# Kernel optimization log

Hardware: AMD Instinct MI355X
Metric: run time of the kernel (lower is better)

The kernel has to match this reference:

```python
import jax, jax.numpy as jnp
import numpy as np

EMB = 64
HEADS = 8
B = 4
T = 2048


def setup_inputs() -> dict:
    key = jax.random.key(0)
    ks = jax.random.split(key, 7)
    s = 0.05
    x = jax.random.normal(ks[0], (B, T, EMB), dtype=jnp.float32)
    y = jax.random.normal(ks[1], (B, T, EMB), dtype=jnp.float32)
    mask = jax.random.randint(ks[2], (1, T, T), 0, 2, dtype=jnp.int32)
    Wk = jax.random.normal(ks[3], (EMB, EMB * HEADS), dtype=jnp.float32) * s
    Wq = jax.random.normal(ks[4], (EMB, EMB * HEADS), dtype=jnp.float32) * s
    Wv = jax.random.normal(ks[5], (EMB, EMB * HEADS), dtype=jnp.float32) * s
    Wu = jax.random.normal(ks[6], (EMB * HEADS, EMB), dtype=jnp.float32) * s
    bu = jnp.zeros((EMB,), dtype=jnp.float32)
    return {"x": x, "y": y, "mask": mask, "Wk": Wk, "Wq": Wq, "Wv": Wv, "Wu": Wu, "bu": bu}


def reference(x, y, mask, Wk, Wq, Wv, Wu, bu):
    b, t_x, e = x.shape
    _, t_y, _ = y.shape
    h = HEADS
    # projections: each head gets full dim e (head_dim == emb in this module)
    k = (x @ Wk).reshape(b, t_x, h, e).transpose(0, 2, 1, 3)  # [b,h,t_x,e]
    q = (y @ Wq).reshape(b, t_y, h, e).transpose(0, 2, 1, 3)  # [b,h,t_y,e]
    v = (x @ Wv).reshape(b, t_x, h, e).transpose(0, 2, 1, 3)  # [b,h,t_x,e]
    scale = jnp.asarray(e, x.dtype) ** 0.25
    q = q / scale
    k = k / scale
    dot = jnp.einsum('bhqe,bhke->bhqk', q, k)  # [b,h,t_y,t_x]
    # mask: [1,t_y,t_x] broadcast over batch*heads; fill -1e9 where mask==0
    dot = jnp.where(mask[:, None, :, :] == 0, jnp.asarray(-1e9, dot.dtype), dot)
    att = jax.nn.softmax(dot, axis=-1)
    out = jnp.einsum('bhqk,bhke->bqhe', att, v).reshape(b, t_y, h * e)
    return out @ Wu + bu
```

## Files before the change

kernel.cpp:

```cpp
#include <hip/hip_runtime.h>

#define EMB 64
#define HEADS 8
#define SEQ 2048

typedef short short8 __attribute__((ext_vector_type(8)));
typedef float f32x4 __attribute__((ext_vector_type(4)));
typedef unsigned int u32;

__device__ __forceinline__ float4 ld4(const float* p) { return *(const float4*)p; }
__device__ __forceinline__ unsigned short f2bf(float f) {
  union { float f; unsigned u; } x; x.f = f;
  return (unsigned short)((x.u + 0x7fffu + ((x.u >> 16) & 1u)) >> 16);
}
__device__ __forceinline__ float bf2f(unsigned short s) {
  union { unsigned u; float f; } x; x.u = ((unsigned)s) << 16;
  return x.f;
}
__device__ __forceinline__ float bits2f(u32 u) {
  union { u32 u; float f; } x; x.u = u;
  return x.f;
}
__device__ __forceinline__ u32 cvtpk(float lo, float hi) {
  u32 r;
  asm("v_cvt_pk_bf16_f32 %0, %1, %2" : "=v"(r) : "v"(lo), "v"(hi));
  return r;
}
__device__ __forceinline__ float vexp2(float x) {
  float r;
  asm("v_exp_f32 %0, %1" : "=v"(r) : "v"(x));
  return r;
}
__device__ __forceinline__ void gload16(const void* g, void* l) {
  __builtin_amdgcn_global_load_lds((const __attribute__((address_space(1))) unsigned int*)g,
                                   (__attribute__((address_space(3))) unsigned int*)l, 16, 0, 0);
}

#define LOG2E 1.4426950408889634f
#define NC0  (-5.770780163555854f)

__global__ __launch_bounds__(256) void prep_kernel(
    const float* __restrict__ x, const float* __restrict__ y,
    const float* __restrict__ Wk, const float* __restrict__ Wq, const float* __restrict__ Wv,
    const int* __restrict__ mask, const float* __restrict__ Wu,
    unsigned short* __restrict__ Kbuf, unsigned short* __restrict__ Qbuf,
    unsigned short* __restrict__ VbufT, u32* __restrict__ pmask,
    unsigned short* __restrict__ WuThi, unsigned short* __restrict__ WuTlo)
{
  __shared__ alignas(16) char psmem[18688];
  const int t = threadIdx.x;
  const int z = blockIdx.z;

  if (z == 3) {
    int (*Ms)[68] = (int (*)[68])psmem;
    const int bid = blockIdx.x * 8 + blockIdx.y;
    const int qblk = bid >> 5, kt = bid & 31;
    #pragma unroll
    for (int j = 0; j < 4; ++j) {
      const int idx = t + j * 256;
      const int row = idx >> 4, col4 = (idx & 15) << 2;
      *(int4*)&Ms[row][col4] =
          *(const int4*)&mask[(size_t)(qblk*64 + row) * SEQ + kt*64 + col4];
    }
    __syncthreads();
    #pragma unroll
    for (int it = 0; it < 8; ++it) {
      const int gid = bid * 2048 + it * 256 + t;
      const int i = gid & 7, ll = (gid >> 3) & 63, ww = (gid >> 9) & 3;
      const int ql = ww*16 + (ll & 15);
      const int g = ll >> 4, c = i >> 1, rr = i & 1;
      const int kl = 16*c + 4*g + 2*rr;
      const int m0 = Ms[ql][kl], m1 = Ms[ql][kl + 1];
      pmask[gid] = (m0 ? 0xFFFFu : 0u) | (m1 ? 0xFFFF0000u : 0u);
    }
    if (blockIdx.y == 7) {
      const int idx = blockIdx.x * 256 + t;
      const int k = idx >> 6, n = idx & 63;
      const float wv = Wu[(size_t)k * EMB + n];
      const unsigned short hi = f2bf(wv);
      const unsigned short lo = f2bf(wv - bf2f(hi));
      WuThi[(size_t)n * 512 + k] = hi;
      WuTlo[(size_t)n * 512 + k] = lo;
    }
    return;
  }

  const int rowblk = blockIdx.x;
  const int h = blockIdx.y;
  const float* __restrict__ W = (z == 0) ? Wk : (z == 1) ? Wv : Wq;
  const float* __restrict__ Ain = (z == 2) ? y : x;

  unsigned short* const WhT = (unsigned short*)psmem;
  unsigned short* const WlT = WhT + 64*72;
  #pragma unroll
  for (int j = 0; j < 4; ++j) {
    const int idx = t + j * 256;
    const int k = idx >> 4, n4 = (idx & 15) << 2;
    const float4 wv = ld4(&W[(size_t)k * (EMB*HEADS) + h*EMB + n4]);
    #pragma unroll
    for (int d = 0; d < 4; ++d) {
      const float v = (d==0)?wv.x:(d==1)?wv.y:(d==2)?wv.z:wv.w;
      const unsigned short hi = f2bf(v);
      WhT[(n4 + d)*72 + k] = hi;
      WlT[(n4 + d)*72 + k] = f2bf(v - bf2f(hi));
    }
  }
  __syncthreads();

  const int wv_ = t >> 6, l = t & 63, g = l >> 4, q15 = l & 15;
  const int b = rowblk >> 5, bh = b * HEADS + h;
  const int trow0 = rowblk * 64 + wv_ * 16;
  const int tloc0 = (rowblk & 31) * 64 + wv_ * 16;
  const f32x4 z4 = (f32x4){0.f,0.f,0.f,0.f};

  short8 xh[2], xl[2];
  #pragma unroll
  for (int kt = 0; kt < 2; ++kt) {
    const float* ap = &Ain[(size_t)(trow0 + q15)*64 + kt*32 + g*8];
    const float4 a0 = ld4(ap), a1 = ld4(ap + 4);
    #pragma unroll
    for (int j = 0; j < 8; ++j) {
      const float v = (j<4) ? ((j==0)?a0.x:(j==1)?a0.y:(j==2)?a0.z:a0.w)
                            : ((j==4)?a1.x:(j==5)?a1.y:(j==6)?a1.z:a1.w);
      const unsigned short hi = f2bf(v);
      xh[kt][j] = (short)hi;
      xl[kt][j] = (short)f2bf(v - bf2f(hi));
    }
  }

  if (z != 1) {
    f32x4 acc[4];
    #pragma unroll
    for (int nt = 0; nt < 4; ++nt) {
      acc[nt] = z4;
      #pragma unroll
      for (int kt = 0; kt < 2; ++kt) {
        const short8 bh_ = *(const short8*)&WhT[(nt*16 + q15)*72 + kt*32 + g*8];
        const short8 bl_ = *(const short8*)&WlT[(nt*16 + q15)*72 + kt*32 + g*8];
        acc[nt] = __builtin_amdgcn_mfma_f32_16x16x32_bf16(xh[kt], bh_, acc[nt], 0,0,0);
        acc[nt] = __builtin_amdgcn_mfma_f32_16x16x32_bf16(xh[kt], bl_, acc[nt], 0,0,0);
        acc[nt] = __builtin_amdgcn_mfma_f32_16x16x32_bf16(xl[kt], bh_, acc[nt], 0,0,0);
      }
    }
    const float scale = (z == 2) ? 0.125f : 1.0f;
    unsigned short* __restrict__ dst = (z == 0) ? Kbuf : Qbuf;
    #pragma unroll
    for (int nt = 0; nt < 4; ++nt)
      #pragma unroll
      for (int r = 0; r < 4; ++r)
        dst[((size_t)bh*SEQ + tloc0 + 4*g + r)*64 + nt*16 + q15] = f2bf(acc[nt][r] * scale);
  } else {
    f32x4 acc[4];
    #pragma unroll
    for (int mt = 0; mt < 4; ++mt) {
      acc[mt] = z4;
      #pragma unroll
      for (int kt = 0; kt < 2; ++kt) {
        const short8 ah_ = *(const short8*)&WhT[(mt*16 + q15)*72 + kt*32 + g*8];
        const short8 al_ = *(const short8*)&WlT[(mt*16 + q15)*72 + kt*32 + g*8];
        acc[mt] = __builtin_amdgcn_mfma_f32_16x16x32_bf16(ah_, xh[kt], acc[mt], 0,0,0);
        acc[mt] = __builtin_amdgcn_mfma_f32_16x16x32_bf16(al_, xh[kt], acc[mt], 0,0,0);
        acc[mt] = __builtin_amdgcn_mfma_f32_16x16x32_bf16(ah_, xl[kt], acc[mt], 0,0,0);
      }
    }
    #pragma unroll
    for (int mt = 0; mt < 4; ++mt)
      #pragma unroll
      for (int r = 0; r < 4; ++r)
        VbufT[((size_t)bh*EMB + mt*16 + 4*g + r)*SEQ + tloc0 + q15] = f2bf(acc[mt][r]);
  }
}

__global__ __launch_bounds__(256, 4) void flash_kernel(
    const unsigned short* __restrict__ Qbuf, const unsigned short* __restrict__ Kbuf,
    const unsigned short* __restrict__ VbufT, const u32* __restrict__ Pmask,
    unsigned short* __restrict__ Oint)
{
  __shared__ alignas(16) char smem[40960];
  char* const K0 = smem;
  char* const K1 = smem + 8192;
  char* const V0 = smem + 16384;
  char* const V1 = smem + 24576;

  const int t = threadIdx.x;
  const int w = t >> 6, l = t & 63, g = l >> 4, q = l & 15;
  const int id = blockIdx.x;
  const int k_ = id >> 3;
  const int bh = (id & 7) * 4 + (k_ >> 5);
  const int qblk = k_ & 31;
  const int b = bh >> 3, h = bh & 7;

  short8 qf[2];
  {
    const unsigned short* qp = Qbuf + ((size_t)bh*SEQ + qblk*64 + w*16 + q)*EMB + g*8;
    qf[0] = *(const short8*)qp;
    qf[1] = *(const short8*)(qp + 32);
  }

  f32x4 oacc[4];
  #pragma unroll
  for (int c = 0; c < 4; ++c) oacc[c] = (f32x4){0.f,0.f,0.f,0.f};
  const f32x4 z4 = (f32x4){0.f,0.f,0.f,0.f};
  float lsum = 0.f;

  char* const Pw = smem + 32768 + w*2048;
  const int sw = (q & 7) << 4;

  const u32* mp = Pmask + ((size_t)(qblk*128 + w))*512 + l*8;

  const int unit0 = w*64 + l, unit1 = 256 + w*64 + l;
  const int row0 = unit0 >> 3, row1 = unit1 >> 3;
  const int gs0 = (unit0 & 7) ^ (row0 & 7), gs1 = (unit1 & 7) ^ (row1 & 7);
  const unsigned short* kp0 = Kbuf + ((size_t)bh*SEQ + row0)*EMB + gs0*8;
  const unsigned short* kp1 = Kbuf + ((size_t)bh*SEQ + row1)*EMB + gs1*8;
  const unsigned short* vp0 = VbufT + ((size_t)bh*EMB + row0)*SEQ + gs0*8;
  const unsigned short* vp1 = VbufT + ((size_t)bh*EMB + row1)*SEQ + gs1*8;

  #define STAGE(KDST, VDST) do {                                                      \
    gload16(kp0, (KDST) + (w*64)*16);                                                 \
    gload16(vp0, (VDST) + (w*64)*16);                                                 \
    gload16(kp1, (KDST) + (256 + w*64)*16);                                           \
    gload16(vp1, (VDST) + (256 + w*64)*16);                                           \
    kp0 += 64*EMB; kp1 += 64*EMB; vp0 += 64; vp1 += 64;                               \
  } while (0)

  STAGE(K0, V0);
  __syncthreads();

  uint4 mw0 = *(const uint4*)mp;
  uint4 mw1 = *(const uint4*)(mp + 4);
  mp += 2048;

  #define TILE(kbase, vbase, DOSTAGE, nkdst, nvdst) do {                               \
    f32x4 sacc[4];                                                                     \
    __builtin_amdgcn_s_setprio(1);                                                     \
    _Pragma("unroll") for (int c = 0; c < 4; ++c) {                                    \
      const short8 kf0 = *(const short8*)((kbase) + (16*c + q)*128 + ((g<<4) ^ sw));   \
      const short8 kf1 = *(const short8*)((kbase) + (16*c + q)*128 + (((4+g)<<4) ^ sw));\
      sacc[c] = __builtin_amdgcn_mfma_f32_16x16x32_bf16(kf0, qf[0], z4, 0,0,0);        \
      sacc[c] = __builtin_amdgcn_mfma_f32_16x16x32_bf16(kf1, qf[1], sacc[c], 0,0,0);   \
    }                                                                                  \
    __builtin_amdgcn_s_setprio(0);                                                     \
    if (DOSTAGE) { STAGE(nkdst, nvdst); }           \
    uint4 mn0 = mw0, mn1 = mw1;                                                        \
    if (DOSTAGE) { mn0 = *(const uint4*)mp; mn1 = *(const uint4*)(mp + 4); mp += 2048; } \
    u32 pw[8];                                                                         \
    _Pragma("unroll") for (int c = 0; c < 4; ++c) {                                    \
      const float p0 = vexp2(fmaf(sacc[c][0], LOG2E, NC0));                            \
      const float p1 = vexp2(fmaf(sacc[c][1], LOG2E, NC0));                            \
      const float p2 = vexp2(fmaf(sacc[c][2], LOG2E, NC0));                            \
      const float p3 = vexp2(fmaf(sacc[c][3], LOG2E, NC0));                            \
      pw[2*c]   = cvtpk(p0, p1);                                                       \
      pw[2*c+1] = cvtpk(p2, p3);                                                       \
    }                                                                                  \
    pw[0] &= mw0.x; pw[1] &= mw0.y; pw[2] &= mw0.z; pw[3] &= mw0.w;                    \
    pw[4] &= mw1.x; pw[5] &= mw1.y; pw[6] &= mw1.z; pw[7] &= mw1.w;                    \
    _Pragma("unroll") for (int c = 0; c < 4; ++c)                                      \
      *(uint2*)(Pw + ((q*128 + 32*c + 8*g) ^ sw)) = make_uint2(pw[2*c], pw[2*c+1]);    \
    float ts = 0.f;                                                                    \
    _Pragma("unroll") for (int i = 0; i < 8; ++i)                                      \
      ts += bits2f(pw[i] << 16) + bits2f(pw[i] & 0xFFFF0000u);                         \
    ts += __shfl_xor(ts, 16);                                                          \
    ts += __shfl_xor(ts, 32);                                                          \
    lsum += ts;                                                                        \
    __builtin_amdgcn_sched_barrier(0);     \
    short8 pf[2];                                                                      \
    pf[0] = *(const short8*)(Pw + ((q*128 + 16*g) ^ sw));                              \
    pf[1] = *(const short8*)(Pw + ((q*128 + 64 + 16*g) ^ sw));                         \
    __builtin_amdgcn_s_setprio(1);                                                     \
    _Pragma("unroll") for (int c = 0; c < 4; ++c) {                                    \
      const short8 vf0 = *(const short8*)((vbase) + (16*c + q)*128 + ((g<<4) ^ sw));   \
      const short8 vf1 = *(const short8*)((vbase) + (16*c + q)*128 + (((4+g)<<4) ^ sw));\
      oacc[c] = __builtin_amdgcn_mfma_f32_16x16x32_bf16(pf[0], vf0, oacc[c], 0,0,0);   \
      oacc[c] = __builtin_amdgcn_mfma_f32_16x16x32_bf16(pf[1], vf1, oacc[c], 0,0,0);   \
    }                                                                                  \
    __builtin_amdgcn_s_setprio(0);                                                     \
    mw0 = mn0; mw1 = mn1;                                                              \
    __syncthreads();     \
  } while (0)

  #pragma unroll 1
  for (int kt2 = 0; kt2 < 16; ++kt2) {
    TILE(K0, V0, true,       K1, V1);
    TILE(K1, V1, (kt2 < 15), K0, V0);
  }
  #undef TILE
  #undef STAGE

  #pragma unroll
  for (int r = 0; r < 4; ++r) {
    const float lr = __shfl(lsum, (l & 48) | (4*g + r));
    const float inv = (lr > 1e-30f) ? 1.f / lr : 0.f;
    #pragma unroll
    for (int c = 0; c < 4; ++c) {
      Oint[((size_t)b*SEQ + qblk*64 + w*16 + 4*g + r)*(EMB*HEADS) + h*EMB + q + 16*c] =
          f2bf(oacc[c][r] * inv);
    }
  }
}

__global__ __launch_bounds__(128) void outproj_kernel(
    const unsigned short* __restrict__ Oint, const unsigned short* __restrict__ WuThi,
    const unsigned short* __restrict__ WuTlo, const float* __restrict__ bu,
    float* __restrict__ out)
{
  const int t = threadIdx.x;
  const int w = t >> 6, l = t & 63, g = l >> 4, q15 = l & 15;
  const int t0 = (blockIdx.x * 2 + w) * 16;
  const f32x4 z4 = (f32x4){0.f,0.f,0.f,0.f};
  f32x4 acc[4] = {z4, z4, z4, z4};

  #pragma unroll 2
  for (int kt = 0; kt < 16; ++kt) {
    const short8 af = *(const short8*)&Oint[(size_t)(t0 + q15)*512 + kt*32 + g*8];
    #pragma unroll
    for (int nt = 0; nt < 4; ++nt) {
      const short8 bh_ = *(const short8*)&WuThi[(size_t)(nt*16 + q15)*512 + kt*32 + g*8];
      const short8 bl_ = *(const short8*)&WuTlo[(size_t)(nt*16 + q15)*512 + kt*32 + g*8];
      acc[nt] = __builtin_amdgcn_mfma_f32_16x16x32_bf16(af, bh_, acc[nt], 0,0,0);
      acc[nt] = __builtin_amdgcn_mfma_f32_16x16x32_bf16(af, bl_, acc[nt], 0,0,0);
    }
  }

  #pragma unroll
  for (int nt = 0; nt < 4; ++nt) {
    const float bv = bu[nt*16 + q15];
    #pragma unroll
    for (int r = 0; r < 4; ++r)
      out[(size_t)(t0 + 4*g + r)*EMB + nt*16 + q15] = acc[nt][r] + bv;
  }
}

extern "C" void kernel_launch(void* const* d_in, const int* in_sizes, int n_in,
                              void* d_out, int out_size, void* d_ws, size_t ws_size,
                              hipStream_t stream) {
  const float* x   = (const float*)d_in[0];
  const float* y   = (const float*)d_in[1];
  const int*   mask= (const int*)d_in[2];
  const float* Wk  = (const float*)d_in[3];
  const float* Wq  = (const float*)d_in[4];
  const float* Wv  = (const float*)d_in[5];
  const float* Wu  = (const float*)d_in[6];
  const float* bu  = (const float*)d_in[7];
  float* out = (float*)d_out;

  unsigned short* Qbuf  = (unsigned short*)d_ws;
  unsigned short* Kbuf  = Qbuf + (size_t)32*SEQ*EMB;
  unsigned short* VbufT = Kbuf + (size_t)32*SEQ*EMB;
  u32* Pmask = (u32*)((char*)d_ws + (size_t)24*1024*1024);
  unsigned short* Oint  = (unsigned short*)((char*)d_ws + (size_t)32*1024*1024);
  unsigned short* WuThi = (unsigned short*)((char*)d_ws + (size_t)40*1024*1024);
  unsigned short* WuTlo = WuThi + 32768;

  prep_kernel<<<dim3(128, 8, 4), 256, 0, stream>>>(x, y, Wk, Wq, Wv, mask, Wu,
                                                   Kbuf, Qbuf, VbufT, Pmask, WuThi, WuTlo);
  flash_kernel<<<1024, 256, 0, stream>>>(Qbuf, Kbuf, VbufT, Pmask, Oint);
  outproj_kernel<<<256, 128, 0, stream>>>(Oint, WuThi, WuTlo, bu, out);
}
```

Measured before the change: 91.59 us.

## Process two 16-row query tiles per wave to reuse K/V fragments

Each wave now handles 32 query rows (two 16-row sub-tiles A and B) instead of 16, so each block covers 128 query rows and the grid halves to 512 blocks. K and V fragments read from LDS are reused across both sub-tiles, which halves K/V LDS reads and global staging per unit of work. The cost is higher register pressure (launch bounds lowered to 2 blocks per CU), a larger shared buffer for P, and fewer blocks to spread across CUs.

```diff
diff --git a/kernel.cpp b/kernel.cpp
--- a/kernel.cpp
+++ b/kernel.cpp
@@ -171,12 +171,12 @@
   }
 }
 
-__global__ __launch_bounds__(256, 4) void flash_kernel(
+__global__ __launch_bounds__(256, 2) void flash_kernel(
     const unsigned short* __restrict__ Qbuf, const unsigned short* __restrict__ Kbuf,
     const unsigned short* __restrict__ VbufT, const u32* __restrict__ Pmask,
     unsigned short* __restrict__ Oint)
 {
-  __shared__ alignas(16) char smem[40960];
+  __shared__ alignas(16) char smem[49152];
   char* const K0 = smem;
   char* const K1 = smem + 8192;
   char* const V0 = smem + 16384;
@@ -186,27 +186,36 @@
   const int w = t >> 6, l = t & 63, g = l >> 4, q = l & 15;
   const int id = blockIdx.x;
   const int k_ = id >> 3;
-  const int bh = (id & 7) * 4 + (k_ >> 5);
-  const int qblk = k_ & 31;
+  const int bh = (id & 7) * 4 + (k_ >> 4);
+  const int qb2 = k_ & 15;
   const int b = bh >> 3, h = bh & 7;
-
-  short8 qf[2];
+  const int rowA = qb2*128 + w*32;
+
+  short8 qfA[2], qfB[2];
   {
-    const unsigned short* qp = Qbuf + ((size_t)bh*SEQ + qblk*64 + w*16 + q)*EMB + g*8;
-    qf[0] = *(const short8*)qp;
-    qf[1] = *(const short8*)(qp + 32);
-  }
-
-  f32x4 oacc[4];
-  #pragma unroll
-  for (int c = 0; c < 4; ++c) oacc[c] = (f32x4){0.f,0.f,0.f,0.f};
+    const unsigned short* qpA = Qbuf + ((size_t)bh*SEQ + rowA + q)*EMB + g*8;
+    qfA[0] = *(const short8*)qpA;
+    qfA[1] = *(const short8*)(qpA + 32);
+    const unsigned short* qpB = qpA + 16*EMB;
+    qfB[0] = *(const short8*)qpB;
+    qfB[1] = *(const short8*)(qpB + 32);
+  }
+
+  f32x4 oaccA[4], oaccB[4];
+  #pragma unroll
+  for (int c = 0; c < 4; ++c) {
+    oaccA[c] = (f32x4){0.f,0.f,0.f,0.f};
+    oaccB[c] = (f32x4){0.f,0.f,0.f,0.f};
+  }
   const f32x4 z4 = (f32x4){0.f,0.f,0.f,0.f};
-  float lsum = 0.f;
-
-  char* const Pw = smem + 32768 + w*2048;
+  float lsumA = 0.f, lsumB = 0.f;
+
+  char* const PwA = smem + 32768 + w*4096;
+  char* const PwB = PwA + 2048;
   const int sw = (q & 7) << 4;
 
-  const u32* mp = Pmask + ((size_t)(qblk*128 + w))*512 + l*8;
+  const int qblk64 = qb2*2 + (w >> 1);
+  const u32* mp = Pmask + ((size_t)(qblk64*128 + (w & 1)*2))*512 + l*8;
 
   const int unit0 = w*64 + l, unit1 = 256 + w*64 + l;
   const int row0 = unit0 >> 3, row1 = unit1 >> 3;
@@ -229,53 +238,80 @@
 
   uint4 mw0 = *(const uint4*)mp;
   uint4 mw1 = *(const uint4*)(mp + 4);
+  uint4 mw2 = *(const uint4*)(mp + 512);
+  uint4 mw3 = *(const uint4*)(mp + 516);
   mp += 2048;
 
   #define TILE(kbase, vbase, DOSTAGE, nkdst, nvdst) do {                               \
-    f32x4 sacc[4];                                                                     \
+    f32x4 saccA[4], saccB[4];                                                          \
     __builtin_amdgcn_s_setprio(1);                                                     \
     _Pragma("unroll") for (int c = 0; c < 4; ++c) {                                    \
       const short8 kf0 = *(const short8*)((kbase) + (16*c + q)*128 + ((g<<4) ^ sw));   \
       const short8 kf1 = *(const short8*)((kbase) + (16*c + q)*128 + (((4+g)<<4) ^ sw));\
-      sacc[c] = __builtin_amdgcn_mfma_f32_16x16x32_bf16(kf0, qf[0], z4, 0,0,0);        \
-      sacc[c] = __builtin_amdgcn_mfma_f32_16x16x32_bf16(kf1, qf[1], sacc[c], 0,0,0);   \
+      saccA[c] = __builtin_amdgcn_mfma_f32_16x16x32_bf16(kf0, qfA[0], z4, 0,0,0);      \
+      saccA[c] = __builtin_amdgcn_mfma_f32_16x16x32_bf16(kf1, qfA[1], saccA[c], 0,0,0);\
+      saccB[c] = __builtin_amdgcn_mfma_f32_16x16x32_bf16(kf0, qfB[0], z4, 0,0,0);      \
+      saccB[c] = __builtin_amdgcn_mfma_f32_16x16x32_bf16(kf1, qfB[1], saccB[c], 0,0,0);\
     }                                                                                  \
     __builtin_amdgcn_s_setprio(0);                                                     \
     if (DOSTAGE) { STAGE(nkdst, nvdst); }           \
-    uint4 mn0 = mw0, mn1 = mw1;                                                        \
-    if (DOSTAGE) { mn0 = *(const uint4*)mp; mn1 = *(const uint4*)(mp + 4); mp += 2048; } \
-    u32 pw[8];                                                                         \
+    uint4 mn0 = mw0, mn1 = mw1, mn2 = mw2, mn3 = mw3;                                  \
+    if (DOSTAGE) {                                                                     \
+      mn0 = *(const uint4*)mp; mn1 = *(const uint4*)(mp + 4);                          \
+      mn2 = *(const uint4*)(mp + 512); mn3 = *(const uint4*)(mp + 516);                \
+      mp += 2048;                                                                      \
+    }                                                                                  \
+    u32 pwA[8], pwB[8];                                                                \
     _Pragma("unroll") for (int c = 0; c < 4; ++c) {                                    \
-      const float p0 = vexp2(fmaf(sacc[c][0], LOG2E, NC0));                            \
-      const float p1 = vexp2(fmaf(sacc[c][1], LOG2E, NC0));                            \
-      const float p2 = vexp2(fmaf(sacc[c][2], LOG2E, NC0));                            \
-      const float p3 = vexp2(fmaf(sacc[c][3], LOG2E, NC0));                            \
-      pw[2*c]   = cvtpk(p0, p1);                                                       \
-      pw[2*c+1] = cvtpk(p2, p3);                                                       \
-    }                                                                                  \
-    pw[0] &= mw0.x; pw[1] &= mw0.y; pw[2] &= mw0.z; pw[3] &= mw0.w;                    \
-    pw[4] &= mw1.x; pw[5] &= mw1.y; pw[6] &= mw1.z; pw[7] &= mw1.w;                    \
-    _Pragma("unroll") for (int c = 0; c < 4; ++c)                                      \
-      *(uint2*)(Pw + ((q*128 + 32*c + 8*g) ^ sw)) = make_uint2(pw[2*c], pw[2*c+1]);    \
-    float ts = 0.f;                                                                    \
-    _Pragma("unroll") for (int i = 0; i < 8; ++i)                                      \
-      ts += bits2f(pw[i] << 16) + bits2f(pw[i] & 0xFFFF0000u);                         \
-    ts += __shfl_xor(ts, 16);                                                          \
-    ts += __shfl_xor(ts, 32);                                                          \
-    lsum += ts;                                                                        \
+      const float a0 = vexp2(fmaf(saccA[c][0], LOG2E, NC0));                           \
+      const float a1 = vexp2(fmaf(saccA[c][1], LOG2E, NC0));                           \
+      const float a2 = vexp2(fmaf(saccA[c][2], LOG2E, NC0));                           \
+      const float a3 = vexp2(fmaf(saccA[c][3], LOG2E, NC0));                           \
+      pwA[2*c]   = cvtpk(a0, a1);                                                      \
+      pwA[2*c+1] = cvtpk(a2, a3);                                                      \
+      const float b0 = vexp2(fmaf(saccB[c][0], LOG2E, NC0));                           \
+      const float b1 = vexp2(fmaf(saccB[c][1], LOG2E, NC0));                           \
+      const float b2 = vexp2(fmaf(saccB[c][2], LOG2E, NC0));                           \
+      const float b3 = vexp2(fmaf(saccB[c][3], LOG2E, NC0));                           \
+      pwB[2*c]   = cvtpk(b0, b1);                                                      \
+      pwB[2*c+1] = cvtpk(b2, b3);                                                      \
+    }                                                                                  \
+    pwA[0] &= mw0.x; pwA[1] &= mw0.y; pwA[2] &= mw0.z; pwA[3] &= mw0.w;                \
+    pwA[4] &= mw1.x; pwA[5] &= mw1.y; pwA[6] &= mw1.z; pwA[7] &= mw1.w;                \
+    pwB[0] &= mw2.x; pwB[1] &= mw2.y; pwB[2] &= mw2.z; pwB[3] &= mw2.w;                \
+    pwB[4] &= mw3.x; pwB[5] &= mw3.y; pwB[6] &= mw3.z; pwB[7] &= mw3.w;                \
+    _Pragma("unroll") for (int c = 0; c < 4; ++c) {                                    \
+      *(uint2*)(PwA + ((q*128 + 32*c + 8*g) ^ sw)) = make_uint2(pwA[2*c], pwA[2*c+1]); \
+      *(uint2*)(PwB + ((q*128 + 32*c + 8*g) ^ sw)) = make_uint2(pwB[2*c], pwB[2*c+1]); \
+    }                                                                                  \
+    float tsA = 0.f, tsB = 0.f;                                                        \
+    _Pragma("unroll") for (int i = 0; i < 8; ++i) {                                    \
+      tsA += bits2f(pwA[i] << 16) + bits2f(pwA[i] & 0xFFFF0000u);                      \
+      tsB += bits2f(pwB[i] << 16) + bits2f(pwB[i] & 0xFFFF0000u);                      \
+    }                                                                                  \
+    tsA += __shfl_xor(tsA, 16);                                                        \
+    tsA += __shfl_xor(tsA, 32);                                                        \
+    tsB += __shfl_xor(tsB, 16);                                                        \
+    tsB += __shfl_xor(tsB, 32);                                                        \
+    lsumA += tsA;                                                                      \
+    lsumB += tsB;                                                                      \
     __builtin_amdgcn_sched_barrier(0);     \
-    short8 pf[2];                                                                      \
-    pf[0] = *(const short8*)(Pw + ((q*128 + 16*g) ^ sw));                              \
-    pf[1] = *(const short8*)(Pw + ((q*128 + 64 + 16*g) ^ sw));                         \
+    short8 pfA[2], pfB[2];                                                             \
+    pfA[0] = *(const short8*)(PwA + ((q*128 + 16*g) ^ sw));                            \
+    pfA[1] = *(const short8*)(PwA + ((q*128 + 64 + 16*g) ^ sw));                       \
+    pfB[0] = *(const short8*)(PwB + ((q*128 + 16*g) ^ sw));                            \
+    pfB[1] = *(const short8*)(PwB + ((q*128 + 64 + 16*g) ^ sw));                       \
     __builtin_amdgcn_s_setprio(1);                                                     \
     _Pragma("unroll") for (int c = 0; c < 4; ++c) {                                    \
       const short8 vf0 = *(const short8*)((vbase) + (16*c + q)*128 + ((g<<4) ^ sw));   \
       const short8 vf1 = *(const short8*)((vbase) + (16*c + q)*128 + (((4+g)<<4) ^ sw));\
-      oacc[c] = __builtin_amdgcn_mfma_f32_16x16x32_bf16(pf[0], vf0, oacc[c], 0,0,0);   \
-      oacc[c] = __builtin_amdgcn_mfma_f32_16x16x32_bf16(pf[1], vf1, oacc[c], 0,0,0);   \
+      oaccA[c] = __builtin_amdgcn_mfma_f32_16x16x32_bf16(pfA[0], vf0, oaccA[c], 0,0,0);\
+      oaccA[c] = __builtin_amdgcn_mfma_f32_16x16x32_bf16(pfA[1], vf1, oaccA[c], 0,0,0);\
+      oaccB[c] = __builtin_amdgcn_mfma_f32_16x16x32_bf16(pfB[0], vf0, oaccB[c], 0,0,0);\
+      oaccB[c] = __builtin_amdgcn_mfma_f32_16x16x32_bf16(pfB[1], vf1, oaccB[c], 0,0,0);\
     }                                                                                  \
     __builtin_amdgcn_s_setprio(0);                                                     \
-    mw0 = mn0; mw1 = mn1;                                                              \
+    mw0 = mn0; mw1 = mn1; mw2 = mn2; mw3 = mn3;                                        \
     __syncthreads();     \
   } while (0)
 
@@ -289,12 +325,16 @@
 
   #pragma unroll
   for (int r = 0; r < 4; ++r) {
-    const float lr = __shfl(lsum, (l & 48) | (4*g + r));
-    const float inv = (lr > 1e-30f) ? 1.f / lr : 0.f;
+    const float lrA = __shfl(lsumA, (l & 48) | (4*g + r));
+    const float invA = (lrA > 1e-30f) ? 1.f / lrA : 0.f;
+    const float lrB = __shfl(lsumB, (l & 48) | (4*g + r));
+    const float invB = (lrB > 1e-30f) ? 1.f / lrB : 0.f;
     #pragma unroll
     for (int c = 0; c < 4; ++c) {
-      Oint[((size_t)b*SEQ + qblk*64 + w*16 + 4*g + r)*(EMB*HEADS) + h*EMB + q + 16*c] =
-          f2bf(oacc[c][r] * inv);
+      Oint[((size_t)b*SEQ + rowA + 4*g + r)*(EMB*HEADS) + h*EMB + q + 16*c] =
+          f2bf(oaccA[c][r] * invA);
+      Oint[((size_t)b*SEQ + rowA + 16 + 4*g + r)*(EMB*HEADS) + h*EMB + q + 16*c] =
+          f2bf(oaccB[c][r] * invB);
     }
   }
 }
@@ -354,6 +394,6 @@
 
   prep_kernel<<<dim3(128, 8, 4), 256, 0, stream>>>(x, y, Wk, Wq, Wv, mask, Wu,
                                                    Kbuf, Qbuf, VbufT, Pmask, WuThi, WuTlo);
-  flash_kernel<<<1024, 256, 0, stream>>>(Qbuf, Kbuf, VbufT, Pmask, Oint);
+  flash_kernel<<<512, 256, 0, stream>>>(Qbuf, Kbuf, VbufT, Pmask, Oint);
   outproj_kernel<<<256, 128, 0, stream>>>(Oint, WuThi, WuTlo, bu, out);
 }
```

After: 85.12 us. 7.1% less time.
